# Kernel optimization log

Hardware: AMD Instinct MI355X
Metric: run time of the kernel (lower is better)

## Reference

```python
import jax, jax.numpy as jnp
import numpy as np

B, T, S, H, C, E, V, OOV = 8, 16, 400, 512, 512, 128, 50000, 50


def setup_inputs() -> dict:
    key = jax.random.key(0)
    ks = jax.random.split(key, 24)
    rn = lambda k, shape, s=0.05: jax.random.normal(k, shape, dtype=jnp.float32) * s
    inp = {
        'input_embeddings': rn(ks[0], (B, T, E), 1.0),
        'context': rn(ks[1], (B, 1, C), 1.0),
        'h0': rn(ks[2], (1, B, H), 1.0),
        'c0': rn(ks[3], (1, B, H), 1.0),
        'encoder_outputs': rn(ks[4], (B, S, C), 1.0),
        'encoder_masks': jnp.ones((B, S), jnp.float32),
        'extra_zeros': jnp.zeros((B, OOV), jnp.float32),
        'extended_source_idx': jax.random.randint(ks[5], (B, S), 0, V + OOV),
        'coverage': jnp.zeros((B, 1, S), jnp.float32),
        # LSTM (single layer), torch gate order i,f,g,o
        'W_ih': rn(ks[6], (4 * H, E)), 'W_hh': rn(ks[7], (4 * H, H)),
        'b_ih': rn(ks[8], (4 * H,)), 'b_hh': rn(ks[9], (4 * H,)),
        # attention (concat + coverage)
        'cov_w': rn(ks[10], (H, 1)),
        'energy_w': rn(ks[11], (H, H + C)), 'energy_b': rn(ks[12], (H,)),
        'v': jax.random.uniform(ks[13], (H,), jnp.float32),
        # projections
        'xctx_w': rn(ks[14], (E, E + C)), 'xctx_b': rn(ks[15], (E,)),
        'attnd_w': rn(ks[16], (H, H + C)), 'attnd_b': rn(ks[17], (H,)),
        'vocab_w': rn(ks[18], (V, H)), 'vocab_b': rn(ks[19], (V,)),
        'pgen_w': rn(ks[20], (1, C + H + E)), 'pgen_b': rn(ks[21], (1,)),
    }
    return inp


def reference(input_embeddings, context, h0, c0, encoder_outputs, encoder_masks,
              extra_zeros, extended_source_idx, coverage,
              W_ih, W_hh, b_ih, b_hh, cov_w, energy_w, energy_b, v,
              xctx_w, xctx_b, attnd_w, attnd_b, vocab_w, vocab_b, pgen_w, pgen_b):
    Bn = input_embeddings.shape[0]
    Sn = encoder_outputs.shape[1]
    bidx = jnp.arange(Bn)[:, None]

    def step(carry, emb_t):
        h, c, ctx, cov = carry  # [B,H],[B,H],[B,C],[B,S]
        x = jnp.concatenate([emb_t, ctx], -1) @ xctx_w.T + xctx_b  # [B,E]
        gates = x @ W_ih.T + b_ih + h @ W_hh.T + b_hh
        i, f, g, o = jnp.split(gates, 4, axis=-1)
        c_new = jax.nn.sigmoid(f) * c + jax.nn.sigmoid(i) * jnp.tanh(g)
        h_new = jax.nn.sigmoid(o) * jnp.tanh(c_new)  # [B,H]
        # concat-style Luong attention with coverage
        cov_proj = cov[..., None] * cov_w[:, 0]  # [B,S,H] (Linear(1,H) no bias)
        cat = jnp.concatenate([
            jnp.broadcast_to(h_new[:, None, :], (Bn, Sn, h_new.shape[-1])),
            encoder_outputs], -1)  # [B,S,H+C]
        energy = jnp.tanh(cat @ energy_w.T + energy_b + cov_proj)
        e = energy @ v  # [B,S]
        probs = jax.nn.softmax(e, -1) * encoder_masks
        probs = probs / (probs.sum(-1, keepdims=True) + 1e-12)
        ctx_new = jnp.einsum('bs,bsc->bc', probs, encoder_outputs)
        cov_new = cov + probs
        vocab_dist = jax.nn.softmax(
            (jnp.concatenate([h_new, ctx_new], -1) @ attnd_w.T + attnd_b) @ vocab_w.T + vocab_b, -1)
        p_gen = jax.nn.sigmoid(jnp.concatenate([ctx_new, h_new, x], -1) @ pgen_w.T + pgen_b)  # [B,1]
        ext = jnp.concatenate([vocab_dist * p_gen, extra_zeros], 1)  # [B,V+OOV]
        final = ext.at[bidx, extended_source_idx].add((1.0 - p_gen) * probs)
        return (h_new, c_new, ctx_new, cov_new), (final, probs, cov_new, p_gen)

    init = (h0[0], c0[0], context[:, 0], coverage[:, 0])
    (h, c, ctx, cov), (finals, attns, covs, pgens) = jax.lax.scan(
        step, init, jnp.swapaxes(input_embeddings, 0, 1))
    final_vocab_dists = jnp.swapaxes(finals, 0, 1)  # [B,T,V+OOV]
    attn_dists = jnp.swapaxes(attns, 0, 1)          # [B,T,S]
    coverages = jnp.swapaxes(covs, 0, 1)            # [B,T,S]
    return (final_vocab_dists, ctx[:, None, :], h[None], c[None], attn_dists, pgens[-1], coverages)
```

## Files before the change

### kernel.cpp

```cpp
#include <hip/hip_runtime.h>
#include <math.h>

#define BB 8
#define TT 16
#define SS 400
#define HH 512
#define EE 128
#define VV 50000
#define VE 50050
#define OOVn 50

#define O1 6406400
#define O2 6410496
#define O3 6414592
#define O4 6418688
#define O5 6469888
#define O6 6469896

#define G_OFF    0
#define EWHB_OFF 1179648
#define ENCG_OFF 1310720
#define WXF_OFF  4600000
#define ENCP_OFF 4600000
#define PM_OFF   5700000

typedef __attribute__((ext_vector_type(4))) float floatx4;
typedef __attribute__((ext_vector_type(8))) short short8;
typedef __attribute__((ext_vector_type(8))) unsigned short ushort8_t;
typedef __attribute__((ext_vector_type(4))) unsigned short ushort4_t;

__device__ __forceinline__ float sigm(float x){ return 1.0f/(1.0f+__expf(-x)); }
__device__ __forceinline__ float ftanh(float x){
  float e = __expf(2.0f*x); return 1.0f - 2.0f/(e + 1.0f);
}
__device__ __forceinline__ unsigned short f2bf(float f){
  union { float f; unsigned int u; } v; v.f = f;
  unsigned int u = v.u;
  return (unsigned short)((u + 0x7FFFu + ((u >> 16) & 1u)) >> 16);
}
__device__ __forceinline__ float bfu(unsigned short u){
  union { unsigned int i; float f; } v; v.i = ((unsigned int)u) << 16; return v.f;
}

__global__ __launch_bounds__(256)
void gemm_bt(const float* __restrict__ A, int lda,
             const float* __restrict__ Bm, int ldb,
             const float* __restrict__ bias,
             float* __restrict__ Cm, int ldc,
             int N, int K, int permute, int obf,
             long bsB, long bsC)
{
  __shared__ unsigned short Ash[128*72];
  __shared__ unsigned short Bsh[64*72];
  int tid = threadIdx.x;
  int mbase = blockIdx.x * 128;
  int nbase = blockIdx.y * 64;
  long z = blockIdx.z;
  const float* Bz = Bm + z*bsB;
  int wave = tid >> 6, lane = tid & 63;
  int wm = (wave & 1) * 64, wn = (wave >> 1) * 32;
  int fl = lane & 15, quad = lane >> 4;

  floatx4 acc[4][2];
  for (int i=0;i<4;i++) for(int j=0;j<2;j++) acc[i][j] = (floatx4)(0.0f);

  for (int kc = 0; kc < K; kc += 64) {
    float4 ra[8], rb[4];
#pragma unroll
    for (int i = 0; i < 8; ++i) {
      int idx = tid + i*256;
      int row = idx >> 4;
      int c4 = (idx & 15) << 2;
      ra[i] = *(const float4*)(A + (size_t)(mbase+row)*lda + kc + c4);
    }
#pragma unroll
    for (int i = 0; i < 4; ++i) {
      int idx = tid + i*256;
      int row = idx >> 4;
      int c4 = (idx & 15) << 2;
      int gn = nbase + row;
      if (gn < N) rb[i] = *(const float4*)(Bz + (size_t)gn*ldb + kc + c4);
      else { rb[i].x = 0.f; rb[i].y = 0.f; rb[i].z = 0.f; rb[i].w = 0.f; }
    }
    __syncthreads();
#pragma unroll
    for (int i = 0; i < 8; ++i) {
      int idx = tid + i*256;
      int o = (idx >> 4)*72 + ((idx & 15) << 2);
      Ash[o+0]=f2bf(ra[i].x); Ash[o+1]=f2bf(ra[i].y); Ash[o+2]=f2bf(ra[i].z); Ash[o+3]=f2bf(ra[i].w);
    }
#pragma unroll
    for (int i = 0; i < 4; ++i) {
      int idx = tid + i*256;
      int o = (idx >> 4)*72 + ((idx & 15) << 2);
      Bsh[o+0]=f2bf(rb[i].x); Bsh[o+1]=f2bf(rb[i].y); Bsh[o+2]=f2bf(rb[i].z); Bsh[o+3]=f2bf(rb[i].w);
    }
    __syncthreads();
#pragma unroll
    for (int ks = 0; ks < 2; ++ks) {
      short8 af[4], bfr[2];
      int ko = ks*32 + quad*8;
#pragma unroll
      for (int i=0;i<4;i++) af[i]  = *(const short8*)&Ash[(wm + i*16 + fl)*72 + ko];
#pragma unroll
      for (int j=0;j<2;j++) bfr[j] = *(const short8*)&Bsh[(wn + j*16 + fl)*72 + ko];
#pragma unroll
      for (int i=0;i<4;i++)
#pragma unroll
        for (int j=0;j<2;j++)
          acc[i][j] = __builtin_amdgcn_mfma_f32_16x16x32_bf16(af[i], bfr[j], acc[i][j], 0,0,0);
    }
    __syncthreads();
  }
  for (int i=0;i<4;i++){
    for (int j=0;j<2;j++){
      int nc = nbase + wn + j*16 + fl;
      if (nc >= N) continue;
      float bv = bias ? bias[nc] : 0.0f;
      for (int r=0;r<4;r++){
        int mg = mbase + wm + i*16 + quad*4 + r;
        int orow = permute ? ((mg & 7)*16 + (mg >> 3)) : mg;
        float v = acc[i][j][r] + bv;
        long ci = (long)orow*ldc + nc + z*bsC;
        if (obf) ((unsigned short*)Cm)[ci] = f2bf(v);
        else     Cm[ci] = v;
      }
    }
  }
}

__global__ __launch_bounds__(256)
void gemm_logits(const unsigned short* __restrict__ Abf,
                 const float* __restrict__ Bm, const float* __restrict__ bias,
                 float* __restrict__ out, float* __restrict__ rowsum)
{
  __shared__ unsigned short Ash[128*72];
  __shared__ unsigned short Bsh[64*72];
  __shared__ float rowpart[128];
  int tid = threadIdx.x;
  int nbase = blockIdx.x * 64;
  int wave = tid >> 6, lane = tid & 63;
  int wm = (wave & 1) * 64, wn = (wave >> 1) * 32;
  int fl = lane & 15, quad = lane >> 4;

  floatx4 acc[4][2];
  for (int i=0;i<4;i++) for(int j=0;j<2;j++) acc[i][j] = (floatx4)(0.0f);
  if (tid < 128) rowpart[tid] = 0.f;

  for (int kc = 0; kc < 512; kc += 64) {
    ushort8_t raa[4];
    float4 rb[4];
#pragma unroll
    for (int i = 0; i < 4; ++i) {
      int idx = tid + i*256;
      int row = idx >> 3;
      int c8 = (idx & 7) << 3;
      raa[i] = *(const ushort8_t*)(Abf + (size_t)row*512 + kc + c8);
    }
#pragma unroll
    for (int i = 0; i < 4; ++i) {
      int idx = tid + i*256;
      int row = idx >> 4;
      int c4 = (idx & 15) << 2;
      int gn = nbase + row;
      if (gn < VV) rb[i] = *(const float4*)(Bm + (size_t)gn*512 + kc + c4);
      else { rb[i].x = 0.f; rb[i].y = 0.f; rb[i].z = 0.f; rb[i].w = 0.f; }
    }
    __syncthreads();
#pragma unroll
    for (int i = 0; i < 4; ++i) {
      int idx = tid + i*256;
      int o = (idx >> 3)*72 + ((idx & 7) << 3);
      *(ushort8_t*)&Ash[o] = raa[i];
    }
#pragma unroll
    for (int i = 0; i < 4; ++i) {
      int idx = tid + i*256;
      int o = (idx >> 4)*72 + ((idx & 15) << 2);
      Bsh[o+0]=f2bf(rb[i].x); Bsh[o+1]=f2bf(rb[i].y); Bsh[o+2]=f2bf(rb[i].z); Bsh[o+3]=f2bf(rb[i].w);
    }
    __syncthreads();
#pragma unroll
    for (int ks = 0; ks < 2; ++ks) {
      short8 af[4], bfr[2];
      int ko = ks*32 + quad*8;
#pragma unroll
      for (int i=0;i<4;i++) af[i]  = *(const short8*)&Ash[(wm + i*16 + fl)*72 + ko];
#pragma unroll
      for (int j=0;j<2;j++) bfr[j] = *(const short8*)&Bsh[(wn + j*16 + fl)*72 + ko];
#pragma unroll
      for (int i=0;i<4;i++)
#pragma unroll
        for (int j=0;j<2;j++)
          acc[i][j] = __builtin_amdgcn_mfma_f32_16x16x32_bf16(af[i], bfr[j], acc[i][j], 0,0,0);
    }
    __syncthreads();
  }
  for (int i=0;i<4;i++){
    for (int r=0;r<4;r++){
      int mg = wm + i*16 + quad*4 + r;
      int orow = (mg & 7)*16 + (mg >> 3);
      float rs = 0.f;
      for (int j=0;j<2;j++){
        int nc = nbase + wn + j*16 + fl;
        if (nc < VV) {
          float e = __expf(acc[i][j][r] + bias[nc]);
          out[(size_t)orow*VE + nc] = e;
          rs += e;
        }
      }
      atomicAdd(&rowpart[mg], rs);
    }
  }
  __syncthreads();
  if (tid < 128) {
    int orow = (tid & 7)*16 + (tid >> 3);
    atomicAdd(&rowsum[orow], rowpart[tid]);
  }
}

__global__ __launch_bounds__(256) void p_wx(const float* __restrict__ wih,
    const float* __restrict__ whh, const float* __restrict__ xcw,
    unsigned short* __restrict__ G, float* __restrict__ wxf)
{
  int blk = blockIdx.x, tid = threadIdx.x;
  if (blk < 640) {
    int rt = blk / 10, ct = blk % 10;
    __shared__ float wl[32*128];
    __shared__ float xl[128*64];
    for (int i = tid; i < 4096; i += 256) {
      int r = i >> 7, k = i & 127;
      wl[i] = wih[(size_t)(rt*32+r)*128 + k];
    }
    for (int i = tid; i < 8192; i += 256) {
      int e = i >> 6, c = i & 63;
      xl[i] = xcw[(size_t)e*640 + ct*64 + c];
    }
    __syncthreads();
    for (int o = tid; o < 2048; o += 256) {
      int r = o >> 6, c = o & 63;
      float acc = 0.f;
      for (int e = 0; e < 128; ++e) acc += wl[r*128+e]*xl[e*64+c];
      G[(size_t)(rt*32+r)*1152 + ct*64 + c] = f2bf(acc);
      int col = ct*64 + c;
      if (col >= 128) wxf[(size_t)(rt*32+r)*512 + col - 128] = acc;
    }
  } else {
    int idx = blk - 640;
    for (int q = 0; q < 2; ++q) {
      int n = idx*2048 + q*1024 + tid*4;
      int r = n >> 9, k = n & 511;
      float4 v = *(const float4*)(whh + n);
      ushort4_t s; s[0]=f2bf(v.x); s[1]=f2bf(v.y); s[2]=f2bf(v.z); s[3]=f2bf(v.w);
      *(ushort4_t*)(G + (size_t)r*1152 + 640 + k) = s;
    }
  }
}

__global__ __launch_bounds__(256) void p_small(const float* __restrict__ wih,
    const float* __restrict__ bih, const float* __restrict__ bhh,
    const float* __restrict__ xb, const float* __restrict__ xcw,
    const float* __restrict__ pw, const float* __restrict__ pb,
    float* __restrict__ gb, float* __restrict__ q, float* __restrict__ qb,
    float* __restrict__ d1, float* __restrict__ d2)
{
  int blk = blockIdx.x, tid = threadIdx.x;
  if (blk < 8) {
    __shared__ float xbl[128];
    if (tid < 128) xbl[tid] = xb[tid];
    __syncthreads();
    int r = blk*256 + tid;
    const float* wr = wih + (size_t)r*128;
    float acc = bih[r] + bhh[r];
    for (int e = 0; e < 128; ++e) acc += wr[e]*xbl[e];
    gb[r] = acc;
  } else if (blk < 11) {
    int o = (blk-8)*256 + tid;
    if (o < 640) {
      float acc = 0.f;
      for (int e = 0; e < 128; ++e) acc += pw[1024+e]*xcw[(size_t)e*640 + o];
      q[o] = acc;
    }
  } else {
    if (tid == 0) {
      float acc = 0.f;
      for (int e = 0; e < 128; ++e) acc += pw[1024+e]*xb[e];
      qb[0] = acc + pb[0];
    }
    if (tid < 128) { d1[tid] = 0.f; d2[tid] = 0.f; }
  }
}

__global__ __launch_bounds__(256) void p_cast(const float* __restrict__ ew,
    unsigned short* __restrict__ ewhb)
{
  int blk = blockIdx.x, tid = threadIdx.x;
  for (int q = 0; q < 2; ++q) {
    size_t n = (size_t)blk*2048 + q*1024 + tid*4;
    int p = (int)(n >> 9), k = (int)(n & 511);
    float4 v = *(const float4*)(ew + (size_t)p*1024 + k);
    ushort4_t s; s[0]=f2bf(v.x); s[1]=f2bf(v.y); s[2]=f2bf(v.z); s[3]=f2bf(v.w);
    *(ushort4_t*)(ewhb + n) = s;
  }
}

__global__ __launch_bounds__(256) void s1g(
    const unsigned short* __restrict__ G, const unsigned short* __restrict__ encG,
    const float* __restrict__ gb,
    const float* __restrict__ emb, const float* __restrict__ context,
    const float* __restrict__ h0, const float* __restrict__ c0,
    const float* __restrict__ coverage,
    const float* __restrict__ PM, const float* __restrict__ d1,
    const float* __restrict__ d2,
    float* __restrict__ A1, float* __restrict__ c_cur,
    float* __restrict__ out, int t)
{
  __shared__ float ueh[8][644];
  __shared__ float uc[8][516];
  __shared__ float part[256];
  __shared__ float gl[64];
  __shared__ float invs[8];
  int tid = threadIdx.x, blk = blockIdx.x;

  if (t >= 1 && tid < 8)
    invs[tid] = 1.0f / (d2[(t-1)*8 + tid] + 1e-12f*d1[(t-1)*8 + tid]);
  __syncthreads();

  for (int i = 0; i < 5; ++i) {
    int slot = i*256 + tid;
    int b = slot / 160, sl = slot - b*160;
    if (sl < 32) {
      *(float4*)&ueh[b][sl*4] = *(const float4*)(emb + (size_t)(b*16+t)*128 + sl*4);
    } else {
      int qq = sl - 32;
      const float* hsrc = t ? (A1 + ((size_t)((t-1)*8+b))*1024) : (h0 + b*512);
      *(float4*)&ueh[b][128 + qq*4] = *(const float4*)(hsrc + qq*4);
    }
  }
  if (t == 0) {
    for (int i = 0; i < 4; ++i) {
      int slot = i*256 + tid;
      int b = slot >> 7, sl = slot & 127;
      *(float4*)&uc[b][sl*4] = *(const float4*)(context + b*512 + sl*4);
    }
  } else {
    const float* pmsrc = PM + (size_t)(t-1)*3200;
    for (int i = 0; i < 4; ++i) {
      int slot = i*256 + tid;
      if (slot < 800) {
        int b = slot / 100, sl = slot - b*100;
        float4 p4 = *(const float4*)(pmsrc + b*400 + sl*4);
        float iv = invs[b];
        p4.x *= iv; p4.y *= iv; p4.z *= iv; p4.w *= iv;
        *(float4*)&uc[b][sl*4] = p4;
      }
    }
  }
  __syncthreads();

  if (t >= 1 && blk < 8) {
    int b = blk;
    const float* covprev = (t == 1) ? (coverage + b*400)
                                    : (out + O6 + ((size_t)(b*16 + t-2))*400);
    size_t o = ((size_t)(b*16 + t-1))*400;
    for (int s = tid; s < 400; s += 256) {
      float pr = uc[b][s];
      out[O4 + o + s] = pr;
      out[O6 + o + s] = covprev[s] + pr;
    }
  }

  int dot = tid >> 2, kq = tid & 3;
  int rr = dot >> 3, b = dot & 7;
  int gate = rr >> 1, jj = rr & 1;
  int r = gate*512 + blk*2 + jj;
  const unsigned short* gr = G + (size_t)r*1152;
  float acc = 0.f;
  {
    const unsigned short* gp = gr + kq*8;
    const float* up = &ueh[b][kq*8];
#pragma unroll
    for (int i = 0; i < 4; ++i) {
      ushort8_t w8 = *(const ushort8_t*)(gp + i*32);
      float4 u0 = *(const float4*)(up + i*32);
      float4 u1 = *(const float4*)(up + i*32 + 4);
      acc += bfu(w8[0])*u0.x + bfu(w8[1])*u0.y + bfu(w8[2])*u0.z + bfu(w8[3])*u0.w
           + bfu(w8[4])*u1.x + bfu(w8[5])*u1.y + bfu(w8[6])*u1.z + bfu(w8[7])*u1.w;
    }
  }
  {
    const unsigned short* gp = gr + 640 + kq*8;
    const float* up = &ueh[b][128 + kq*8];
#pragma unroll 4
    for (int i = 0; i < 16; ++i) {
      ushort8_t w8 = *(const ushort8_t*)(gp + i*32);
      float4 u0 = *(const float4*)(up + i*32);
      float4 u1 = *(const float4*)(up + i*32 + 4);
      acc += bfu(w8[0])*u0.x + bfu(w8[1])*u0.y + bfu(w8[2])*u0.z + bfu(w8[3])*u0.w
           + bfu(w8[4])*u1.x + bfu(w8[5])*u1.y + bfu(w8[6])*u1.z + bfu(w8[7])*u1.w;
    }
  }
  if (t == 0) {
    const unsigned short* gp = gr + 128 + kq*8;
    const float* up = &uc[b][kq*8];
#pragma unroll 4
    for (int i = 0; i < 16; ++i) {
      ushort8_t w8 = *(const ushort8_t*)(gp + i*32);
      float4 u0 = *(const float4*)(up + i*32);
      float4 u1 = *(const float4*)(up + i*32 + 4);
      acc += bfu(w8[0])*u0.x + bfu(w8[1])*u0.y + bfu(w8[2])*u0.z + bfu(w8[3])*u0.w
           + bfu(w8[4])*u1.x + bfu(w8[5])*u1.y + bfu(w8[6])*u1.z + bfu(w8[7])*u1.w;
    }
  } else {
    const unsigned short* gp = encG + ((size_t)(b*2048 + r))*400 + kq*8;
    const float* up = &uc[b][kq*8];
#pragma unroll 4
    for (int i = 0; i < 12; ++i) {
      ushort8_t w8 = *(const ushort8_t*)(gp + i*32);
      float4 u0 = *(const float4*)(up + i*32);
      float4 u1 = *(const float4*)(up + i*32 + 4);
      acc += bfu(w8[0])*u0.x + bfu(w8[1])*u0.y + bfu(w8[2])*u0.z + bfu(w8[3])*u0.w
           + bfu(w8[4])*u1.x + bfu(w8[5])*u1.y + bfu(w8[6])*u1.z + bfu(w8[7])*u1.w;
    }
    if (kq < 2) {
      ushort8_t w8 = *(const ushort8_t*)(gp + 12*32);
      float4 u0 = *(const float4*)(up + 12*32);
      float4 u1 = *(const float4*)(up + 12*32 + 4);
      acc += bfu(w8[0])*u0.x + bfu(w8[1])*u0.y + bfu(w8[2])*u0.z + bfu(w8[3])*u0.w
           + bfu(w8[4])*u1.x + bfu(w8[5])*u1.y + bfu(w8[6])*u1.z + bfu(w8[7])*u1.w;
    }
  }
  part[tid] = acc;
  __syncthreads();
  if (tid < 64) {
    int rr2 = tid >> 3;
    int r2 = (rr2 >> 1)*512 + blk*2 + (rr2 & 1);
    gl[tid] = part[tid*4] + part[tid*4+1] + part[tid*4+2] + part[tid*4+3] + gb[r2];
  }
  __syncthreads();
  if (tid < 16) {
    int jj2 = tid >> 3, b2 = tid & 7;
    float gi = gl[(0*2+jj2)*8 + b2];
    float gf = gl[(1*2+jj2)*8 + b2];
    float gg = gl[(2*2+jj2)*8 + b2];
    float go = gl[(3*2+jj2)*8 + b2];
    int j = blk*2 + jj2;
    float cp = t ? c_cur[b2*512+j] : c0[b2*512+j];
    float cn = sigm(gf)*cp + sigm(gi)*ftanh(gg);
    float hn = sigm(go)*ftanh(cn);
    c_cur[b2*512+j] = cn;
    A1[((size_t)(t*8+b2))*1024 + j] = hn;
  }
}

__global__ __launch_bounds__(256) void s2_hp(
    const unsigned short* __restrict__ ewhb, const float* __restrict__ eb,
    const float* __restrict__ A1, float* __restrict__ hp, int t)
{
  __shared__ float hl[8*516];
  __shared__ float part[256];
  int tid = threadIdx.x, pc = blockIdx.x;
  for (int b = 0; b < 8; ++b)
    for (int k = tid; k < 512; k += 256)
      hl[b*516 + k] = A1[((size_t)(t*8+b))*1024 + k];
  __syncthreads();
  int dot = tid >> 2, kq = tid & 3;
  int rr = dot >> 3, b = dot & 7;
  int p = pc*8 + rr;
  const unsigned short* wp = ewhb + (size_t)p*512 + kq*16;
  const float* hh = hl + b*516 + kq*16;
  float acc = 0.f;
#pragma unroll
  for (int i = 0; i < 8; ++i) {
    ushort8_t wa = *(const ushort8_t*)(wp + i*64);
    ushort8_t wb = *(const ushort8_t*)(wp + i*64 + 8);
    float4 h0v = *(const float4*)(hh + i*64);
    float4 h1v = *(const float4*)(hh + i*64 + 4);
    float4 h2v = *(const float4*)(hh + i*64 + 8);
    float4 h3v = *(const float4*)(hh + i*64 + 12);
    acc += bfu(wa[0])*h0v.x + bfu(wa[1])*h0v.y + bfu(wa[2])*h0v.z + bfu(wa[3])*h0v.w
         + bfu(wa[4])*h1v.x + bfu(wa[5])*h1v.y + bfu(wa[6])*h1v.z + bfu(wa[7])*h1v.w
         + bfu(wb[0])*h2v.x + bfu(wb[1])*h2v.y + bfu(wb[2])*h2v.z + bfu(wb[3])*h2v.w
         + bfu(wb[4])*h3v.x + bfu(wb[5])*h3v.y + bfu(wb[6])*h3v.z + bfu(wb[7])*h3v.w;
  }
  part[tid] = acc;
  __syncthreads();
  if (tid < 64) {
    int rr2 = tid >> 3, b2 = tid & 7;
    int p2 = pc*8 + rr2;
    hp[b2*512 + p2] = eb[p2] + part[tid*4] + part[tid*4+1] + part[tid*4+2] + part[tid*4+3];
  }
}

__global__ __launch_bounds__(256) void s3e(
    const unsigned short* __restrict__ encpb, const float* __restrict__ hp,
    const float* __restrict__ vvec, const float* __restrict__ covw,
    const float* __restrict__ masks, const float* __restrict__ coverage,
    const float* __restrict__ out6v, float* __restrict__ PM,
    float* __restrict__ d1, float* __restrict__ d2, int t)
{
  int tid = threadIdx.x;
  int b = blockIdx.x >> 4, sc = blockIdx.x & 15;
  int w = tid >> 6, lane = tid & 63;
  int h0i = lane*8;
  __shared__ float red1[4], red2[4];
  float hpv[8], vv[8], cw[8];
  {
    const float* hpp = hp + b*512 + h0i;
    float4 a0 = *(const float4*)(hpp), a1 = *(const float4*)(hpp+4);
    hpv[0]=a0.x; hpv[1]=a0.y; hpv[2]=a0.z; hpv[3]=a0.w;
    hpv[4]=a1.x; hpv[5]=a1.y; hpv[6]=a1.z; hpv[7]=a1.w;
    float4 v0 = *(const float4*)(vvec+h0i), v1 = *(const float4*)(vvec+h0i+4);
    vv[0]=v0.x; vv[1]=v0.y; vv[2]=v0.z; vv[3]=v0.w;
    vv[4]=v1.x; vv[5]=v1.y; vv[6]=v1.z; vv[7]=v1.w;
    float4 c0v = *(const float4*)(covw+h0i), c1v = *(const float4*)(covw+h0i+4);
    cw[0]=c0v.x; cw[1]=c0v.y; cw[2]=c0v.z; cw[3]=c0v.w;
    cw[4]=c1v.x; cw[5]=c1v.y; cw[6]=c1v.z; cw[7]=c1v.w;
  }
  const float* covp = t ? (out6v + ((size_t)(b*16 + t-1))*400) : (coverage + b*400);
  float a1s = 0.f, a2s = 0.f;
  for (int sl = w; sl < 25; sl += 4) {
    int s = sc*25 + sl;
    float cv = covp[s];
    const unsigned short* ep = encpb + ((size_t)(b*400+s))*512 + h0i;
    ushort8_t e8 = *(const ushort8_t*)ep;
    float acc = 0.f;
#pragma unroll
    for (int i = 0; i < 8; ++i)
      acc += ftanh(hpv[i] + bfu(e8[i]) + cv*cw[i]) * vv[i];
    for (int off = 32; off > 0; off >>= 1) acc += __shfl_down(acc, off);
    if (lane == 0) {
      float pe = __expf(acc);
      float pmv = pe * masks[b*400 + s];
      PM[(size_t)t*3200 + b*400 + s] = pmv;
      a1s += pe; a2s += pmv;
    }
  }
  if (lane == 0) { red1[w] = a1s; red2[w] = a2s; }
  __syncthreads();
  if (tid == 0) {
    atomicAdd(&d1[t*8+b], red1[0]+red1[1]+red1[2]+red1[3]);
    atomicAdd(&d2[t*8+b], red2[0]+red2[1]+red2[2]+red2[3]);
  }
}

__global__ __launch_bounds__(256) void ctx_all(
    const float* __restrict__ PM, const float* __restrict__ d1,
    const float* __restrict__ d2, const float* __restrict__ enc,
    float* __restrict__ A1, float* __restrict__ out)
{
  int tid = threadIdx.x;
  int b = blockIdx.x >> 2, cc = blockIdx.x & 3;
  __shared__ float prl[16][400];
  __shared__ float redbuf[16][128];
  __shared__ float invs[16];
  if (tid < 16) invs[tid] = 1.0f / (d2[tid*8+b] + 1e-12f*d1[tid*8+b]);
  __syncthreads();
  for (int i = 0; i < 7; ++i) {
    int slot = i*256 + tid;
    if (slot < 1600) {
      int tt = slot / 100, sl = slot - tt*100;
      float4 p4 = *(const float4*)(PM + (size_t)tt*3200 + b*400 + sl*4);
      float iv = invs[tt];
      p4.x *= iv; p4.y *= iv; p4.z *= iv; p4.w *= iv;
      *(float4*)&prl[tt][sl*4] = p4;
    }
  }
  __syncthreads();
  if (cc == 0) {
    size_t o15 = ((size_t)(b*16 + 15))*400;
    size_t o14 = ((size_t)(b*16 + 14))*400;
    for (int s = tid; s < 400; s += 256) {
      float pr = prl[15][s];
      out[O4 + o15 + s] = pr;
      out[O6 + o15 + s] = out[O6 + o14 + s] + pr;
    }
  }
  int c = cc*128 + (tid & 127);
  int sg = tid >> 7;
  float acc[16];
#pragma unroll
  for (int tt = 0; tt < 16; ++tt) acc[tt] = 0.f;
  for (int s = sg*200; s < sg*200 + 200; ++s) {
    float ev = enc[((size_t)(b*400 + s))*512 + c];
#pragma unroll
    for (int tt = 0; tt < 16; ++tt) acc[tt] += prl[tt][s]*ev;
  }
  if (sg == 1) {
#pragma unroll
    for (int tt = 0; tt < 16; ++tt) redbuf[tt][tid & 127] = acc[tt];
  }
  __syncthreads();
  if (sg == 0) {
#pragma unroll
    for (int tt = 0; tt < 16; ++tt)
      A1[((size_t)(tt*8+b))*1024 + 512 + c] = acc[tt] + redbuf[tt][tid & 127];
  }
}

__global__ __launch_bounds__(256) void e_pgen(
    const float* __restrict__ A1, const float* __restrict__ c_cur,
    const float* __restrict__ emb, const float* __restrict__ context,
    const float* __restrict__ pw, const float* __restrict__ q,
    const float* __restrict__ qb, float* __restrict__ pgen,
    float* __restrict__ rowsum, float* __restrict__ out)
{
  int blk = blockIdx.x, tid = threadIdx.x;
  if (blk < 128) {
    int m = blk, t = m >> 3, b = m & 7;
    const float* ctxT = A1 + (size_t)m*1024 + 512;
    const float* hT   = A1 + (size_t)m*1024;
    const float* embp = emb + (size_t)(b*16+t)*128;
    const float* ctxP = t ? (A1 + ((size_t)((t-1)*8+b))*1024 + 512) : (context + b*512);
    float acc = 0.f;
    for (int k = tid; k < 512; k += 256)
      acc += pw[k]*ctxT[k] + pw[512+k]*hT[k] + q[128+k]*ctxP[k];
    if (tid < 128) acc += q[tid]*embp[tid];
    for (int off = 32; off > 0; off >>= 1) acc += __shfl_down(acc, off);
    __shared__ float red[4];
    if (!(tid & 63)) red[tid>>6] = acc;
    __syncthreads();
    if (tid == 0) {
      float pg = sigm(red[0]+red[1]+red[2]+red[3] + qb[0]);
      pgen[m] = pg;
      if (t == 15) out[O5 + b] = pg;
    }
  } else if (blk == 128) {
    for (int i = tid; i < 4096; i += 256) {
      int b = i >> 9, j = i & 511;
      out[O1 + i] = A1[((size_t)(120+b))*1024 + 512 + j];
    }
  } else if (blk == 129) {
    for (int i = tid; i < 4096; i += 256) {
      int b = i >> 9, j = i & 511;
      out[O2 + i] = A1[((size_t)(120+b))*1024 + j];
    }
  } else if (blk == 130) {
    for (int i = tid; i < 4096; i += 256) out[O3 + i] = c_cur[i];
  } else {
    if (tid < 128) rowsum[tid] = 0.f;
  }
}

__global__ __launch_bounds__(256) void k_scale(
    float* __restrict__ out, const float* __restrict__ pgen,
    const float* __restrict__ rowsum, const float* __restrict__ ez)
{
  int orow = blockIdx.x, cy = blockIdx.y, tid = threadIdx.x;
  int b = orow >> 4, t = orow & 15;
  float sc = pgen[t*8+b] / rowsum[orow];
  int c0 = cy*6256;
  int c1 = (cy == 7) ? VE : c0 + 6256;
  float* row = out + (size_t)orow*VE;
  for (int c = c0 + tid*4; c < c1; c += 1024) {
    if (c + 4 <= VV && c + 4 <= c1) {
      float4 v = *(float4*)(row + c);
      v.x *= sc; v.y *= sc; v.z *= sc; v.w *= sc;
      *(float4*)(row + c) = v;
    } else {
      for (int e = 0; e < 4; ++e) {
        int cc2 = c + e;
        if (cc2 < c1) row[cc2] = (cc2 < VV) ? row[cc2]*sc : ez[b*OOVn + cc2 - VV];
      }
    }
  }
}

__global__ __launch_bounds__(256) void k_scatter(
    float* __restrict__ out, const float* __restrict__ pgen,
    const int* __restrict__ extidx)
{
  int m = blockIdx.x, tid = threadIdx.x;
  int b = m & 7, t = m >> 3;
  float* row = out + ((size_t)(b*TT + t))*VE;
  float onem = 1.0f - pgen[m];
  const float* pr = out + O4 + ((size_t)(b*TT+t))*SS;
  for (int s = tid; s < SS; s += 256) {
    int ix = extidx[b*SS + s];
    atomicAdd(&row[ix], onem * pr[s]);
  }
}

extern "C" void kernel_launch(void* const* d_in, const int* in_sizes, int n_in,
                              void* d_out, int out_size, void* d_ws, size_t ws_size,
                              hipStream_t stream)
{
  (void)in_sizes; (void)n_in; (void)out_size; (void)ws_size;
  const float* emb      = (const float*)d_in[0];
  const float* context  = (const float*)d_in[1];
  const float* h0       = (const float*)d_in[2];
  const float* c0       = (const float*)d_in[3];
  const float* enc      = (const float*)d_in[4];
  const float* masks    = (const float*)d_in[5];
  const float* ez       = (const float*)d_in[6];
  const int*   extidx   = (const int*)d_in[7];
  const float* coverage = (const float*)d_in[8];
  const float* wih      = (const float*)d_in[9];
  const float* whh      = (const float*)d_in[10];
  const float* bih      = (const float*)d_in[11];
  const float* bhh      = (const float*)d_in[12];
  const float* covw     = (const float*)d_in[13];
  const float* ew       = (const float*)d_in[14];
  const float* eb       = (const float*)d_in[15];
  const float* vvec     = (const float*)d_in[16];
  const float* xw       = (const float*)d_in[17];
  const float* xb       = (const float*)d_in[18];
  const float* aw       = (const float*)d_in[19];
  const float* ab       = (const float*)d_in[20];
  const float* vw       = (const float*)d_in[21];
  const float* vb       = (const float*)d_in[22];
  const float* pw       = (const float*)d_in[23];
  const float* pb       = (const float*)d_in[24];
  float* out = (float*)d_out;

  float* ws = (float*)d_ws;
  float* A1       = ws;
  float* c_cur    = ws + 131072;
  float* hp       = ws + 135168;
  unsigned short* attnd_bf = (unsigned short*)(ws + 139264);
  float* pgen     = ws + 172032;
  float* gb       = ws + 172160;
  float* q        = ws + 174208;
  float* qb       = ws + 174848;
  float* d1       = ws + 174852;
  float* d2       = ws + 174980;
  float* rowsum   = ws + 175108;

  unsigned short* G     = (unsigned short*)(out + G_OFF);
  unsigned short* ewhb  = (unsigned short*)(out + EWHB_OFF);
  unsigned short* encG  = (unsigned short*)(out + ENCG_OFF);
  float*          wxf   = out + WXF_OFF;
  unsigned short* encpb = (unsigned short*)(out + ENCP_OFF);
  float*          PM    = out + PM_OFF;

  p_wx<<<1152, 256, 0, stream>>>(wih, whh, xw, G, wxf);
  p_small<<<12, 256, 0, stream>>>(wih, bih, bhh, xb, xw, pw, pb, gb, q, qb, d1, d2);
  p_cast<<<128, 256, 0, stream>>>(ew, ewhb);
  gemm_bt<<<dim3(16,7,8), 256, 0, stream>>>(wxf, 512, enc, 512,
      (const float*)nullptr, (float*)encG, 400, 400, 512, 0, 1,
      (long)400*512, (long)2048*400);
  gemm_bt<<<dim3(25,8,1), 256, 0, stream>>>(enc, 512, ew + 512, 1024,
      (const float*)nullptr, (float*)encpb, 512, 512, 512, 0, 1, 0, 0);

  for (int t = 0; t < TT; ++t) {
    s1g<<<256, 256, 0, stream>>>(G, encG, gb, emb, context, h0, c0, coverage,
                                 PM, d1, d2, A1, c_cur, out, t);
    s2_hp<<<64, 256, 0, stream>>>(ewhb, eb, A1, hp, t);
    s3e<<<128, 256, 0, stream>>>(encpb, hp, vvec, covw, masks, coverage,
                                 out + O6, PM, d1, d2, t);
  }

  ctx_all<<<32, 256, 0, stream>>>(PM, d1, d2, enc, A1, out);
  e_pgen<<<132, 256, 0, stream>>>(A1, c_cur, emb, context, pw, q, qb, pgen, rowsum, out);
  gemm_bt<<<dim3(1,8,1), 256, 0, stream>>>(A1, 1024, aw, 1024, ab,
      (float*)attnd_bf, 512, 512, 1024, 0, 1, 0, 0);
  gemm_logits<<<782, 256, 0, stream>>>(attnd_bf, vw, vb, out, rowsum);
  k_scale<<<dim3(128,8), 256, 0, stream>>>(out, pgen, rowsum, ez);
  k_scatter<<<128, 256, 0, stream>>>(out, pgen, extidx);
}
```

Before: 802.9 us.

## Load logits GEMM operands directly from global into MFMA registers, skip LDS staging

The vocab logits GEMM no longer stages A and B tiles through shared memory. Each lane now loads its MFMA fragments straight from global memory and converts B from fp32 to bf16 in registers, which removes two barriers per k-chunk and the LDS store/load traffic. The row-sum partials are now reduced with wave shuffles before one shared atomic per 16 lanes, instead of one atomic per lane. In exchange, each A row is re-read by several waves and blocks with less coalesced per-lane access, and there is no prefetch overlap, so performance relies on L1/L2 caching.

Result: slower. 822.3 us (+2.4%).

```diff
diff --git a/kernel.cpp b/kernel.cpp
--- a/kernel.cpp
+++ b/kernel.cpp
@@ -134,8 +134,6 @@
                  const float* __restrict__ Bm, const float* __restrict__ bias,
                  float* __restrict__ out, float* __restrict__ rowsum)
 {
-  __shared__ unsigned short Ash[128*72];
-  __shared__ unsigned short Bsh[64*72];
   __shared__ float rowpart[128];
   int tid = threadIdx.x;
   int nbase = blockIdx.x * 64;
@@ -146,61 +144,51 @@
   floatx4 acc[4][2];
   for (int i=0;i<4;i++) for(int j=0;j<2;j++) acc[i][j] = (floatx4)(0.0f);
   if (tid < 128) rowpart[tid] = 0.f;
+  __syncthreads();
+
+  const unsigned short* Ap = Abf + (size_t)(wm + fl)*512 + quad*8;
+  int gn0 = nbase + wn + fl;
+  int gn1 = gn0 + 16;
+  int gc0 = gn0 < VV ? gn0 : VV - 1;
+  int gc1 = gn1 < VV ? gn1 : VV - 1;
+  const float* Bp0 = Bm + (size_t)gc0*512 + quad*8;
+  const float* Bp1 = Bm + (size_t)gc1*512 + quad*8;
 
   for (int kc = 0; kc < 512; kc += 64) {
-    ushort8_t raa[4];
-    float4 rb[4];
-#pragma unroll
-    for (int i = 0; i < 4; ++i) {
-      int idx = tid + i*256;
-      int row = idx >> 3;
-      int c8 = (idx & 7) << 3;
-      raa[i] = *(const ushort8_t*)(Abf + (size_t)row*512 + kc + c8);
-    }
-#pragma unroll
-    for (int i = 0; i < 4; ++i) {
-      int idx = tid + i*256;
-      int row = idx >> 4;
-      int c4 = (idx & 15) << 2;
-      int gn = nbase + row;
-      if (gn < VV) rb[i] = *(const float4*)(Bm + (size_t)gn*512 + kc + c4);
-      else { rb[i].x = 0.f; rb[i].y = 0.f; rb[i].z = 0.f; rb[i].w = 0.f; }
-    }
-    __syncthreads();
-#pragma unroll
-    for (int i = 0; i < 4; ++i) {
-      int idx = tid + i*256;
-      int o = (idx >> 3)*72 + ((idx & 7) << 3);
-      *(ushort8_t*)&Ash[o] = raa[i];
-    }
-#pragma unroll
-    for (int i = 0; i < 4; ++i) {
-      int idx = tid + i*256;
-      int o = (idx >> 4)*72 + ((idx & 15) << 2);
-      Bsh[o+0]=f2bf(rb[i].x); Bsh[o+1]=f2bf(rb[i].y); Bsh[o+2]=f2bf(rb[i].z); Bsh[o+3]=f2bf(rb[i].w);
-    }
-    __syncthreads();
 #pragma unroll
     for (int ks = 0; ks < 2; ++ks) {
-      short8 af[4], bfr[2];
-      int ko = ks*32 + quad*8;
-#pragma unroll
-      for (int i=0;i<4;i++) af[i]  = *(const short8*)&Ash[(wm + i*16 + fl)*72 + ko];
-#pragma unroll
-      for (int j=0;j<2;j++) bfr[j] = *(const short8*)&Bsh[(wn + j*16 + fl)*72 + ko];
+      int ko = kc + ks*32;
+      short8 af[4];
 #pragma unroll
       for (int i=0;i<4;i++)
-#pragma unroll
-        for (int j=0;j<2;j++)
-          acc[i][j] = __builtin_amdgcn_mfma_f32_16x16x32_bf16(af[i], bfr[j], acc[i][j], 0,0,0);
-    }
-    __syncthreads();
-  }
+        af[i] = *(const short8*)(Ap + (size_t)i*16*512 + ko);
+      float4 x0 = *(const float4*)(Bp0 + ko);
+      float4 x1 = *(const float4*)(Bp0 + ko + 4);
+      float4 y0 = *(const float4*)(Bp1 + ko);
+      float4 y1 = *(const float4*)(Bp1 + ko + 4);
+      short8 bfr[2];
+      bfr[0][0]=(short)f2bf(x0.x); bfr[0][1]=(short)f2bf(x0.y);
+      bfr[0][2]=(short)f2bf(x0.z); bfr[0][3]=(short)f2bf(x0.w);
+      bfr[0][4]=(short)f2bf(x1.x); bfr[0][5]=(short)f2bf(x1.y);
+      bfr[0][6]=(short)f2bf(x1.z); bfr[0][7]=(short)f2bf(x1.w);
+      bfr[1][0]=(short)f2bf(y0.x); bfr[1][1]=(short)f2bf(y0.y);
+      bfr[1][2]=(short)f2bf(y0.z); bfr[1][3]=(short)f2bf(y0.w);
+      bfr[1][4]=(short)f2bf(y1.x); bfr[1][5]=(short)f2bf(y1.y);
+      bfr[1][6]=(short)f2bf(y1.z); bfr[1][7]=(short)f2bf(y1.w);
+#pragma unroll
+      for (int i=0;i<4;i++) {
+        acc[i][0] = __builtin_amdgcn_mfma_f32_16x16x32_bf16(af[i], bfr[0], acc[i][0], 0,0,0);
+        acc[i][1] = __builtin_amdgcn_mfma_f32_16x16x32_bf16(af[i], bfr[1], acc[i][1], 0,0,0);
+      }
+    }
+  }
+
   for (int i=0;i<4;i++){
     for (int r=0;r<4;r++){
       int mg = wm + i*16 + quad*4 + r;
       int orow = (mg & 7)*16 + (mg >> 3);
       float rs = 0.f;
+#pragma unroll
       for (int j=0;j<2;j++){
         int nc = nbase + wn + j*16 + fl;
         if (nc < VV) {
@@ -209,7 +197,11 @@
           rs += e;
         }
       }
-      atomicAdd(&rowpart[mg], rs);
+      rs += __shfl_down(rs, 8);
+      rs += __shfl_down(rs, 4);
+      rs += __shfl_down(rs, 2);
+      rs += __shfl_down(rs, 1);
+      if (fl == 0) atomicAdd(&rowpart[mg], rs);
     }
   }
   __syncthreads();
```

## Compute context vector per step in attention kernel instead of precomputed encoder-gate GEMM

Applied to the files above, without the earlier changes.

Drops the precomputed encoder-projected gate matrix (a batched GEMM of the LSTM input weights through the encoder outputs, 8x2048x400). The attention kernel now accumulates the unnormalized context vector each step with atomics, and the gate kernel consumes the raw context through the original 512-wide weight columns. The separate final ctx_all kernel is removed and its work is folded into e_pgen. This removes a large precompute GEMM and shrinks the per-step weight reads from encG (400 per batch per row) to shared G columns, at the cost of per-step atomics over encoder rows and fp32 atomic summation-order nondeterminism.

New measurement: 771.9 us. 3.9% less time.

```diff
diff --git a/kernel.cpp b/kernel.cpp
--- a/kernel.cpp
+++ b/kernel.cpp
@@ -19,10 +19,9 @@
 
 #define G_OFF    0
 #define EWHB_OFF 1179648
-#define ENCG_OFF 1310720
-#define WXF_OFF  4600000
 #define ENCP_OFF 4600000
 #define PM_OFF   5700000
+#define CTXR_OFF 5800000
 
 typedef __attribute__((ext_vector_type(4))) float floatx4;
 typedef __attribute__((ext_vector_type(8))) short short8;
@@ -221,7 +220,7 @@
 
 __global__ __launch_bounds__(256) void p_wx(const float* __restrict__ wih,
     const float* __restrict__ whh, const float* __restrict__ xcw,
-    unsigned short* __restrict__ G, float* __restrict__ wxf)
+    unsigned short* __restrict__ G)
 {
   int blk = blockIdx.x, tid = threadIdx.x;
   if (blk < 640) {
@@ -242,8 +241,6 @@
       float acc = 0.f;
       for (int e = 0; e < 128; ++e) acc += wl[r*128+e]*xl[e*64+c];
       G[(size_t)(rt*32+r)*1152 + ct*64 + c] = f2bf(acc);
-      int col = ct*64 + c;
-      if (col >= 128) wxf[(size_t)(rt*32+r)*512 + col - 128] = acc;
     }
   } else {
     int idx = blk - 640;
@@ -292,7 +289,7 @@
 }
 
 __global__ __launch_bounds__(256) void p_cast(const float* __restrict__ ew,
-    unsigned short* __restrict__ ewhb)
+    unsigned short* __restrict__ ewhb, float* __restrict__ ctxraw)
 {
   int blk = blockIdx.x, tid = threadIdx.x;
   for (int q = 0; q < 2; ++q) {
@@ -302,16 +299,17 @@
     ushort4_t s; s[0]=f2bf(v.x); s[1]=f2bf(v.y); s[2]=f2bf(v.z); s[3]=f2bf(v.w);
     *(ushort4_t*)(ewhb + n) = s;
   }
+  for (int i = tid; i < 512; i += 256) ctxraw[(size_t)blk*512 + i] = 0.f;
 }
 
 __global__ __launch_bounds__(256) void s1g(
-    const unsigned short* __restrict__ G, const unsigned short* __restrict__ encG,
+    const unsigned short* __restrict__ G,
     const float* __restrict__ gb,
     const float* __restrict__ emb, const float* __restrict__ context,
     const float* __restrict__ h0, const float* __restrict__ c0,
     const float* __restrict__ coverage,
     const float* __restrict__ PM, const float* __restrict__ d1,
-    const float* __restrict__ d2,
+    const float* __restrict__ d2, const float* __restrict__ ctxraw,
     float* __restrict__ A1, float* __restrict__ c_cur,
     float* __restrict__ out, int t)
 {
@@ -337,34 +335,26 @@
       *(float4*)&ueh[b][128 + qq*4] = *(const float4*)(hsrc + qq*4);
     }
   }
-  if (t == 0) {
-    for (int i = 0; i < 4; ++i) {
-      int slot = i*256 + tid;
-      int b = slot >> 7, sl = slot & 127;
-      *(float4*)&uc[b][sl*4] = *(const float4*)(context + b*512 + sl*4);
-    }
-  } else {
-    const float* pmsrc = PM + (size_t)(t-1)*3200;
-    for (int i = 0; i < 4; ++i) {
-      int slot = i*256 + tid;
-      if (slot < 800) {
-        int b = slot / 100, sl = slot - b*100;
-        float4 p4 = *(const float4*)(pmsrc + b*400 + sl*4);
-        float iv = invs[b];
-        p4.x *= iv; p4.y *= iv; p4.z *= iv; p4.w *= iv;
-        *(float4*)&uc[b][sl*4] = p4;
-      }
-    }
+  for (int i = 0; i < 4; ++i) {
+    int slot = i*256 + tid;
+    int b = slot >> 7, sl = slot & 127;
+    const float* csrc = t ? (ctxraw + ((size_t)((t-1)*8+b))*512)
+                          : (context + (size_t)b*512);
+    float4 v = *(const float4*)(csrc + sl*4);
+    if (t) { float iv = invs[b]; v.x*=iv; v.y*=iv; v.z*=iv; v.w*=iv; }
+    *(float4*)&uc[b][sl*4] = v;
   }
   __syncthreads();
 
   if (t >= 1 && blk < 8) {
     int b = blk;
+    float iv = invs[b];
     const float* covprev = (t == 1) ? (coverage + b*400)
                                     : (out + O6 + ((size_t)(b*16 + t-2))*400);
+    const float* pmsrc = PM + (size_t)(t-1)*3200 + b*400;
     size_t o = ((size_t)(b*16 + t-1))*400;
     for (int s = tid; s < 400; s += 256) {
-      float pr = uc[b][s];
+      float pr = pmsrc[s] * iv;
       out[O4 + o + s] = pr;
       out[O6 + o + s] = covprev[s] + pr;
     }
@@ -389,18 +379,6 @@
     }
   }
   {
-    const unsigned short* gp = gr + 640 + kq*8;
-    const float* up = &ueh[b][128 + kq*8];
-#pragma unroll 4
-    for (int i = 0; i < 16; ++i) {
-      ushort8_t w8 = *(const ushort8_t*)(gp + i*32);
-      float4 u0 = *(const float4*)(up + i*32);
-      float4 u1 = *(const float4*)(up + i*32 + 4);
-      acc += bfu(w8[0])*u0.x + bfu(w8[1])*u0.y + bfu(w8[2])*u0.z + bfu(w8[3])*u0.w
-           + bfu(w8[4])*u1.x + bfu(w8[5])*u1.y + bfu(w8[6])*u1.z + bfu(w8[7])*u1.w;
-    }
-  }
-  if (t == 0) {
     const unsigned short* gp = gr + 128 + kq*8;
     const float* up = &uc[b][kq*8];
 #pragma unroll 4
@@ -411,21 +389,15 @@
       acc += bfu(w8[0])*u0.x + bfu(w8[1])*u0.y + bfu(w8[2])*u0.z + bfu(w8[3])*u0.w
            + bfu(w8[4])*u1.x + bfu(w8[5])*u1.y + bfu(w8[6])*u1.z + bfu(w8[7])*u1.w;
     }
-  } else {
-    const unsigned short* gp = encG + ((size_t)(b*2048 + r))*400 + kq*8;
-    const float* up = &uc[b][kq*8];
+  }
+  {
+    const unsigned short* gp = gr + 640 + kq*8;
+    const float* up = &ueh[b][128 + kq*8];
 #pragma unroll 4
-    for (int i = 0; i < 12; ++i) {
+    for (int i = 0; i < 16; ++i) {
       ushort8_t w8 = *(const ushort8_t*)(gp + i*32);
       float4 u0 = *(const float4*)(up + i*32);
       float4 u1 = *(const float4*)(up + i*32 + 4);
-      acc += bfu(w8[0])*u0.x + bfu(w8[1])*u0.y + bfu(w8[2])*u0.z + bfu(w8[3])*u0.w
-           + bfu(w8[4])*u1.x + bfu(w8[5])*u1.y + bfu(w8[6])*u1.z + bfu(w8[7])*u1.w;
-    }
-    if (kq < 2) {
-      ushort8_t w8 = *(const ushort8_t*)(gp + 12*32);
-      float4 u0 = *(const float4*)(up + 12*32);
-      float4 u1 = *(const float4*)(up + 12*32 + 4);
       acc += bfu(w8[0])*u0.x + bfu(w8[1])*u0.y + bfu(w8[2])*u0.z + bfu(w8[3])*u0.w
            + bfu(w8[4])*u1.x + bfu(w8[5])*u1.y + bfu(w8[6])*u1.z + bfu(w8[7])*u1.w;
     }
@@ -496,14 +468,16 @@
     const unsigned short* __restrict__ encpb, const float* __restrict__ hp,
     const float* __restrict__ vvec, const float* __restrict__ covw,
     const float* __restrict__ masks, const float* __restrict__ coverage,
-    const float* __restrict__ out6v, float* __restrict__ PM,
-    float* __restrict__ d1, float* __restrict__ d2, int t)
+    const float* __restrict__ out6v, const float* __restrict__ enc,
+    float* __restrict__ PM, float* __restrict__ d1, float* __restrict__ d2,
+    float* __restrict__ ctxraw, int t)
 {
   int tid = threadIdx.x;
   int b = blockIdx.x >> 4, sc = blockIdx.x & 15;
   int w = tid >> 6, lane = tid & 63;
   int h0i = lane*8;
   __shared__ float red1[4], red2[4];
+  __shared__ float pms[25];
   float hpv[8], vv[8], cw[8];
   {
     const float* hpp = hp + b*512 + h0i;
@@ -533,6 +507,7 @@
       float pe = __expf(acc);
       float pmv = pe * masks[b*400 + s];
       PM[(size_t)t*3200 + b*400 + s] = pmv;
+      pms[sl] = pmv;
       a1s += pe; a2s += pmv;
     }
   }
@@ -542,79 +517,50 @@
     atomicAdd(&d1[t*8+b], red1[0]+red1[1]+red1[2]+red1[3]);
     atomicAdd(&d2[t*8+b], red2[0]+red2[1]+red2[2]+red2[3]);
   }
-}
-
-__global__ __launch_bounds__(256) void ctx_all(
-    const float* __restrict__ PM, const float* __restrict__ d1,
-    const float* __restrict__ d2, const float* __restrict__ enc,
-    float* __restrict__ A1, float* __restrict__ out)
-{
-  int tid = threadIdx.x;
-  int b = blockIdx.x >> 2, cc = blockIdx.x & 3;
-  __shared__ float prl[16][400];
-  __shared__ float redbuf[16][128];
-  __shared__ float invs[16];
-  if (tid < 16) invs[tid] = 1.0f / (d2[tid*8+b] + 1e-12f*d1[tid*8+b]);
-  __syncthreads();
-  for (int i = 0; i < 7; ++i) {
-    int slot = i*256 + tid;
-    if (slot < 1600) {
-      int tt = slot / 100, sl = slot - tt*100;
-      float4 p4 = *(const float4*)(PM + (size_t)tt*3200 + b*400 + sl*4);
-      float iv = invs[tt];
-      p4.x *= iv; p4.y *= iv; p4.z *= iv; p4.w *= iv;
-      *(float4*)&prl[tt][sl*4] = p4;
-    }
-  }
-  __syncthreads();
-  if (cc == 0) {
-    size_t o15 = ((size_t)(b*16 + 15))*400;
-    size_t o14 = ((size_t)(b*16 + 14))*400;
-    for (int s = tid; s < 400; s += 256) {
-      float pr = prl[15][s];
-      out[O4 + o15 + s] = pr;
-      out[O6 + o15 + s] = out[O6 + o14 + s] + pr;
-    }
-  }
-  int c = cc*128 + (tid & 127);
-  int sg = tid >> 7;
-  float acc[16];
-#pragma unroll
-  for (int tt = 0; tt < 16; ++tt) acc[tt] = 0.f;
-  for (int s = sg*200; s < sg*200 + 200; ++s) {
-    float ev = enc[((size_t)(b*400 + s))*512 + c];
-#pragma unroll
-    for (int tt = 0; tt < 16; ++tt) acc[tt] += prl[tt][s]*ev;
-  }
-  if (sg == 1) {
-#pragma unroll
-    for (int tt = 0; tt < 16; ++tt) redbuf[tt][tid & 127] = acc[tt];
-  }
-  __syncthreads();
-  if (sg == 0) {
-#pragma unroll
-    for (int tt = 0; tt < 16; ++tt)
-      A1[((size_t)(tt*8+b))*1024 + 512 + c] = acc[tt] + redbuf[tt][tid & 127];
+  {
+    float acc0 = 0.f, acc1 = 0.f;
+    const float* encb = enc + ((size_t)(b*400 + sc*25))*512;
+#pragma unroll 5
+    for (int sl = 0; sl < 25; ++sl) {
+      float pmv = pms[sl];
+      const float* er = encb + (size_t)sl*512;
+      acc0 += pmv * er[tid];
+      acc1 += pmv * er[tid + 256];
+    }
+    float* cr = ctxraw + ((size_t)(t*8+b))*512;
+    atomicAdd(&cr[tid], acc0);
+    atomicAdd(&cr[tid+256], acc1);
   }
 }
 
 __global__ __launch_bounds__(256) void e_pgen(
-    const float* __restrict__ A1, const float* __restrict__ c_cur,
+    const float* __restrict__ A1f, const float* __restrict__ c_cur,
     const float* __restrict__ emb, const float* __restrict__ context,
     const float* __restrict__ pw, const float* __restrict__ q,
-    const float* __restrict__ qb, float* __restrict__ pgen,
+    const float* __restrict__ qb,
+    const float* __restrict__ d1, const float* __restrict__ d2,
+    const float* __restrict__ ctxraw, const float* __restrict__ PM,
+    float* __restrict__ A1, float* __restrict__ pgen,
     float* __restrict__ rowsum, float* __restrict__ out)
 {
   int blk = blockIdx.x, tid = threadIdx.x;
   if (blk < 128) {
     int m = blk, t = m >> 3, b = m & 7;
-    const float* ctxT = A1 + (size_t)m*1024 + 512;
-    const float* hT   = A1 + (size_t)m*1024;
+    __shared__ float invT, invP;
+    if (tid == 0) invT = 1.0f / (d2[m] + 1e-12f*d1[m]);
+    if (tid == 64) invP = t ? 1.0f / (d2[m-8] + 1e-12f*d1[m-8]) : 0.f;
+    __syncthreads();
+    const float* crT = ctxraw + (size_t)m*512;
+    const float* crP = ctxraw + (size_t)(t ? m-8 : m)*512;
+    const float* hT   = A1f + (size_t)m*1024;
     const float* embp = emb + (size_t)(b*16+t)*128;
-    const float* ctxP = t ? (A1 + ((size_t)((t-1)*8+b))*1024 + 512) : (context + b*512);
     float acc = 0.f;
-    for (int k = tid; k < 512; k += 256)
-      acc += pw[k]*ctxT[k] + pw[512+k]*hT[k] + q[128+k]*ctxP[k];
+    for (int k = tid; k < 512; k += 256) {
+      float cT = crT[k] * invT;
+      float cP = t ? crP[k] * invP : context[(size_t)b*512 + k];
+      acc += pw[k]*cT + pw[512+k]*hT[k] + q[128+k]*cP;
+      A1[(size_t)m*1024 + 512 + k] = cT;
+    }
     if (tid < 128) acc += q[tid]*embp[tid];
     for (int off = 32; off > 0; off >>= 1) acc += __shfl_down(acc, off);
     __shared__ float red[4];
@@ -628,17 +574,29 @@
   } else if (blk == 128) {
     for (int i = tid; i < 4096; i += 256) {
       int b = i >> 9, j = i & 511;
-      out[O1 + i] = A1[((size_t)(120+b))*1024 + 512 + j];
+      float inv = 1.0f / (d2[120+b] + 1e-12f*d1[120+b]);
+      out[O1 + i] = ctxraw[(size_t)(120+b)*512 + j] * inv;
     }
   } else if (blk == 129) {
     for (int i = tid; i < 4096; i += 256) {
       int b = i >> 9, j = i & 511;
-      out[O2 + i] = A1[((size_t)(120+b))*1024 + j];
+      out[O2 + i] = A1f[((size_t)(120+b))*1024 + j];
     }
   } else if (blk == 130) {
     for (int i = tid; i < 4096; i += 256) out[O3 + i] = c_cur[i];
+  } else if (blk == 131) {
+    if (tid < 128) rowsum[tid] = 0.f;
   } else {
-    if (tid < 128) rowsum[tid] = 0.f;
+    int b = blk - 132;
+    float inv = 1.0f / (d2[120+b] + 1e-12f*d1[120+b]);
+    const float* pmsrc = PM + (size_t)15*3200 + b*400;
+    size_t o15 = ((size_t)(b*16 + 15))*400;
+    size_t o14 = ((size_t)(b*16 + 14))*400;
+    for (int s = tid; s < 400; s += 256) {
+      float pr = pmsrc[s] * inv;
+      out[O4 + o15 + s] = pr;
+      out[O6 + o15 + s] = out[O6 + o14 + s] + pr;
+    }
   }
 }
 
@@ -728,30 +686,26 @@
 
   unsigned short* G     = (unsigned short*)(out + G_OFF);
   unsigned short* ewhb  = (unsigned short*)(out + EWHB_OFF);
-  unsigned short* encG  = (unsigned short*)(out + ENCG_OFF);
-  float*          wxf   = out + WXF_OFF;
   unsigned short* encpb = (unsigned short*)(out + ENCP_OFF);
   float*          PM    = out + PM_OFF;
-
-  p_wx<<<1152, 256, 0, stream>>>(wih, whh, xw, G, wxf);
+  float*          ctxr  = out + CTXR_OFF;
+
+  p_wx<<<1152, 256, 0, stream>>>(wih, whh, xw, G);
   p_small<<<12, 256, 0, stream>>>(wih, bih, bhh, xb, xw, pw, pb, gb, q, qb, d1, d2);
-  p_cast<<<128, 256, 0, stream>>>(ew, ewhb);
-  gemm_bt<<<dim3(16,7,8), 256, 0, stream>>>(wxf, 512, enc, 512,
-      (const float*)nullptr, (float*)encG, 400, 400, 512, 0, 1,
-      (long)400*512, (long)2048*400);
+  p_cast<<<128, 256, 0, stream>>>(ew, ewhb, ctxr);
   gemm_bt<<<dim3(25,8,1), 256, 0, stream>>>(enc, 512, ew + 512, 1024,
       (const float*)nullptr, (float*)encpb, 512, 512, 512, 0, 1, 0, 0);
 
   for (int t = 0; t < TT; ++t) {
-    s1g<<<256, 256, 0, stream>>>(G, encG, gb, emb, context, h0, c0, coverage,
-                                 PM, d1, d2, A1, c_cur, out, t);
+    s1g<<<256, 256, 0, stream>>>(G, gb, emb, context, h0, c0, coverage,
+                                 PM, d1, d2, ctxr, A1, c_cur, out, t);
     s2_hp<<<64, 256, 0, stream>>>(ewhb, eb, A1, hp, t);
     s3e<<<128, 256, 0, stream>>>(encpb, hp, vvec, covw, masks, coverage,
-                                 out + O6, PM, d1, d2, t);
-  }
-
-  ctx_all<<<32, 256, 0, stream>>>(PM, d1, d2, enc, A1, out);
-  e_pgen<<<132, 256, 0, stream>>>(A1, c_cur, emb, context, pw, q, qb, pgen, rowsum, out);
+                                 out + O6, enc, PM, d1, d2, ctxr, t);
+  }
+
+  e_pgen<<<140, 256, 0, stream>>>(A1, c_cur, emb, context, pw, q, qb,
+                                  d1, d2, ctxr, PM, A1, pgen, rowsum, out);
   gemm_bt<<<dim3(1,8,1), 256, 0, stream>>>(A1, 1024, aw, 1024, ab,
       (float*)attnd_bf, 512, 512, 1024, 0, 1, 0, 0);
   gemm_logits<<<782, 256, 0, stream>>>(attnd_bf, vw, vb, out, rowsum);
```
